# Optimization experiments

Measured on AMD Instinct MI355X. Metric: run time of the kernel, lower is better.

The kernel has to match this reference:

```python
import jax, jax.numpy as jnp
import numpy as np

B, H, W = 16, 512, 512
HW = H * W
K = 512  # max regions kept per image (compacted region list for jit)


def _ccl(mask):
    """8-connected component labeling on a (H,W) bool mask.
    Label = min flat pixel index of the component (matches skimage scan-order
    region ordering after compaction); background label = HW sentinel."""
    idx = jnp.arange(HW, dtype=jnp.int32).reshape(H, W)
    lab0 = jnp.where(mask, idx, HW)

    def body(c):
        l, _ = c
        p = jnp.pad(l, 1, constant_values=HW)
        m = l
        for dr in (-1, 0, 1):
            for dc in (-1, 0, 1):
                m = jnp.minimum(m, p[1 + dr:1 + dr + H, 1 + dc:1 + dc + W])
        nl = jnp.where(mask, m, HW)
        return nl, jnp.all(nl == l)

    lab, _ = jax.lax.while_loop(lambda c: ~c[1], body, (lab0, jnp.array(False)))
    return lab


def _pixel_errors(pred_m, gt_m):
    """Faithful vectorized version of TopoLoss.calculate_error for one image.
    All torch updates are max-semantics (set-to-1 or raise-to-error), so the
    final map is an elementwise max over region contributions."""
    pl = _ccl(pred_m).ravel()  # pred labels, bg = HW
    gl = _ccl(gt_m).ravel()    # gt labels, bg = HW
    ones = jnp.ones(HW, jnp.float32)
    rows = (jnp.arange(HW) // W).astype(jnp.float32)
    cols = (jnp.arange(HW) % W).astype(jnp.float32)
    seg = lambda v, l: jax.ops.segment_sum(v, l, num_segments=HW + 1)
    pa, psr, psc = seg(ones, pl), seg(rows, pl), seg(cols, pl)
    ga, gsr, gsc = seg(ones, gl), seg(rows, gl), seg(cols, gl)
    p_valid = pa[:HW] > 0
    g_valid = ga[:HW] > 0
    # compact region lists; stable argsort keeps ascending label order = scan order
    p_ids = jnp.argsort(jnp.where(p_valid, 0, 1))[:K]
    g_ids = jnp.argsort(jnp.where(g_valid, 0, 1))[:K]
    pv, gv = p_valid[p_ids], g_valid[g_ids]
    pA, gA = pa[p_ids], ga[g_ids]
    pcr, pcc = psr[p_ids] / jnp.maximum(pA, 1.0), psc[p_ids] / jnp.maximum(pA, 1.0)
    gcr, gcc = gsr[g_ids] / jnp.maximum(gA, 1.0), gsc[g_ids] / jnp.maximum(gA, 1.0)
    # nearest gt centroid per pred region (argmin ties -> first, as in torch loop)
    d2 = (pcr[:, None] - gcr[None, :]) ** 2 + (pcc[:, None] - gcc[None, :]) ** 2
    d2 = jnp.where(gv[None, :], d2, jnp.inf)
    nn = jnp.argmin(d2, axis=1)  # (K,) compact gt index
    ratio = 1.0 - gA[nn] / jnp.maximum(pA, 1.0)
    e = jnp.minimum(jnp.abs(1.0 - jnp.exp(ratio)), 1.0)
    gt_f = gt_m.astype(jnp.float32).ravel()
    pr_f = pred_m.astype(jnp.float32).ravel()
    # per-region overlap flags (check_overlap)
    ov_p = jax.ops.segment_max(gt_f, pl, num_segments=HW + 1) > 0
    ov_g = jax.ops.segment_max(pr_f, gl, num_segments=HW + 1) > 0
    has_gt = jnp.any(g_valid)
    e_eff = jnp.where(pv & ov_p[p_ids] & has_gt, e, 0.0)
    e_full = jnp.zeros(HW + 1, jnp.float32).at[p_ids].set(e_eff)
    # max error among overlapping pred regions matched to each gt region
    e_gt = jnp.maximum(
        jax.ops.segment_max(jnp.where(e_eff > 0, e_eff, -1.0), nn, num_segments=K), 0.0)
    e_gt_full = jnp.zeros(HW + 1, jnp.float32).at[g_ids].set(jnp.where(gv, e_gt, 0.0))
    in_p = pl < HW
    in_g = gl < HW
    err = jnp.where(in_p & ~has_gt, 1.0, 0.0)                                   # no gt regions
    err = jnp.where(in_p & has_gt & ~ov_p[pl], 1.0, err)                        # pred region w/o overlap
    err = jnp.maximum(err, jnp.where(in_p & has_gt & ov_p[pl] & (gt_f != 1.0),
                                     e_full[pl], 0.0))                          # pred pixels, gt!=1
    err = jnp.maximum(err, jnp.where(in_g & (pr_f < 1.0), e_gt_full[gl], 0.0))  # matched gt pixels, pred<1
    err = jnp.where(in_g & ~ov_g[gl], 1.0, err)                                 # gt region w/o overlap
    return err.reshape(H, W)


def _forward(inputs, target):
    score = jax.nn.sigmoid(inputs)  # forward() applies sigmoid before _topo_loss
    pred = score > 0.5
    gt = target > 0.5
    pe = jax.lax.stop_gradient(jax.vmap(_pixel_errors)(pred, gt))
    loss_map = (jax.nn.sigmoid((score + 1.0) * pe) - 0.5) * 2.0
    loss = jnp.mean(loss_map)
    m1 = 1.0 - jnp.mean(pe)
    m2 = 1.0 - jnp.sum(pe) / jnp.count_nonzero(pe).astype(jnp.float32)
    return loss, m1, m2


def setup_inputs() -> dict:
    key = jax.random.key(0)
    k1, k2 = jax.random.split(key)
    # low-frequency fields -> realistic blob regions after thresholding
    inputs = 3.0 * jax.image.resize(jax.random.normal(k1, (B, 16, 16)), (B, H, W), "cubic")
    target = (jax.image.resize(jax.random.normal(k2, (B, 16, 16)), (B, H, W), "cubic") > 0).astype(jnp.float32)
    return {"inputs": inputs, "target": target, "epoch": 1}


def reference(inputs, target, epoch):
    return _forward(inputs, target)
```

## Files before the change

kernel.cpp:

```cpp
#include <hip/hip_runtime.h>

#define NB 16
#define HH 512
#define WW 512
#define HWN (HH * WW)
#define SENT HWN
#define KC 512
#define RCAP 4096
#define CCAP 4096
#define PN (NB * HWN)
#define TPB 256
#define IMAX 0x7FFFFFFF
#define TS 64
#define TSQ (TS * TS)
#define NFIN (NB * 64)

typedef unsigned short ushortT;
typedef unsigned int uintT;
typedef unsigned long long ullT;

__device__ __forceinline__ int findRootL(int* s, int i) {
    int p = s[i];
    while (p != i) { i = p; p = s[i]; }
    return i;
}

__device__ __forceinline__ void uniteL(int* s, int a, int b) {
    int ra = findRootL(s, a);
    int rb = findRootL(s, b);
    while (ra != rb) {
        int lo = min(ra, rb), hi = max(ra, rb);
        int old = atomicMin(&s[hi], lo);
        if (old == hi) return;
        ra = old; rb = lo;
    }
}

__device__ __forceinline__ int rootPk(const int* __restrict__ par, int s) {
    int q = par[s];
    while ((q & (CCAP - 1)) != s) { s = q & (CCAP - 1); q = par[s]; }
    return q;
}

__device__ __forceinline__ void uniteS(int* par, int a, int b) {
    int pa = rootPk(par, a);
    int pb = rootPk(par, b);
    while (pa != pb) {
        int lo = min(pa, pb), hi = max(pa, pb);
        int hs = hi & (CCAP - 1);
        int old = atomicMin(&par[hs], lo);
        if (old == hi) return;
        pa = rootPk(par, old & (CCAP - 1));
        pb = rootPk(par, lo & (CCAP - 1));
    }
}

__device__ __forceinline__ int bsearch_k(const int* a, int key) {
    int lo = 0, hi = KC;
    while (lo < hi) { int m = (lo + hi) >> 1; if (a[m] < key) lo = m + 1; else hi = m; }
    return (lo < KC && a[lo] == key) ? lo : -1;
}

__global__ __launch_bounds__(TPB) void k_prep(const float* __restrict__ in, const float* __restrict__ tg,
                                              ullT* __restrict__ rmP, ullT* __restrict__ rmG) {
    int lane = threadIdx.x & 63;
    int wid = (blockIdx.x * blockDim.x + threadIdx.x) >> 6;
    const float4* in4 = (const float4*)in;
    const float4* tg4 = (const float4*)tg;
    #pragma unroll
    for (int it = 0; it < 2; it++) {
        int span = wid + (it << 13);
        int vidx = (span << 6) + lane;
        float4 a = in4[vidx];
        float4 t4 = tg4[vidx];
        uintT bp = (a.x > 0.0f) | ((a.y > 0.0f) << 1) | ((a.z > 0.0f) << 2) | ((a.w > 0.0f) << 3);
        uintT bg = (t4.x > 0.5f) | ((t4.y > 0.5f) << 1) | ((t4.z > 0.5f) << 2) | ((t4.w > 0.5f) << 3);
        ullT vp = (ullT)bp << ((lane & 15) << 2);
        ullT vg = (ullT)bg << ((lane & 15) << 2);
        #pragma unroll
        for (int o = 1; o < 16; o <<= 1) {
            vp |= __shfl_xor(vp, o);
            vg |= __shfl_xor(vg, o);
        }
        if ((lane & 15) == 0) {
            int g = (span << 8) + ((lane >> 4) << 6);
            int b = g >> 18, r = (g >> 9) & 511, tc = (g >> 6) & 7;
            int idx = (((tc << 4) + b) << 9) + r;
            rmP[idx] = vp; rmG[idx] = vg;
        }
    }
}

__global__ __launch_bounds__(TPB) void k_local(const ullT* __restrict__ rmPArr, const ullT* __restrict__ rmGArr,
                        ushortT* __restrict__ slotP, ushortT* __restrict__ slotG,
                        int* __restrict__ parP, int* __restrict__ parG,
                        ullT* __restrict__ cmLP, ullT* __restrict__ cmRP,
                        ullT* __restrict__ cmLG, ullT* __restrict__ cmRG,
                        int* __restrict__ candCntP, int* __restrict__ candCntG,
                        int* __restrict__ sAreaP, int* __restrict__ sRP, int* __restrict__ sCP, int* __restrict__ sOvP,
                        int* __restrict__ sAreaG, int* __restrict__ sRG, int* __restrict__ sCG, int* __restrict__ sOvG) {
    __shared__ int s[TSQ];
    __shared__ ullT rm[TS], rmO[TS];
    int side = blockIdx.x & 1;
    int tileIdx = blockIdx.x >> 1;
    int b = tileIdx >> 6;
    int tile = tileIdx & 63;
    int r0 = (tile >> 3) << 6, c0 = (tile & 7) << 6;
    int tc = tile & 7;
    int base = (b << 18) + (r0 << 9) + c0;
    int wv = threadIdx.x >> 6, lane = threadIdx.x & 63;

    const ullT* own = side ? rmGArr : rmPArr;
    const ullT* oth = side ? rmPArr : rmGArr;
    ushortT* slotArr = side ? slotG : slotP;
    int* par  = side ? parG : parP;
    ullT* cmLo = side ? cmLG : cmLP;
    ullT* cmRo = side ? cmRG : cmRP;
    int* candCnt = side ? candCntG : candCntP;
    int* sArea = side ? sAreaG : sAreaP;
    int* sR = side ? sRG : sRP;
    int* sC = side ? sCG : sCP;
    int* sOv = side ? sOvG : sOvP;

    int rowIdx = (((tc << 4) + b) << 9) + r0;
    if (threadIdx.x < 64) rm[threadIdx.x] = own[rowIdx + threadIdx.x];
    else if (threadIdx.x < 128) rmO[threadIdx.x - 64] = oth[rowIdx + threadIdx.x - 64];
    __syncthreads();

    if (threadIdx.x < 64) {
        ullT v = rm[threadIdx.x];
        ullT mL = __ballot((v & 1ULL) != 0);
        ullT mR = __ballot((v >> 63) != 0);
        if (threadIdx.x == 0) { cmLo[tileIdx] = mL; cmRo[tileIdx] = mR; }
    }

    #pragma unroll
    for (int k = 0; k < 16; k++) {
        int lr = wv + (k << 2);
        ullT mp = rm[lr];
        bool p = (mp >> lane) & 1ULL;
        int t = (lr << 6) + lane;
        ullT below = (lane == 0) ? 0ULL : ((~mp) & ((1ULL << lane) - 1ULL));
        int st = below ? (64 - __clzll(below)) : 0;
        s[t] = p ? ((lr << 6) + st) : TSQ;
    }
    __syncthreads();

    for (int lr = wv; lr < TS; lr += 4) {
        if (lr == 0) continue;
        int t = (lr << 6) + lane;
        ullT m = rm[lr], a = rm[lr - 1];
        if ((m >> lane) & 1ULL) {
            bool N  = (a >> lane) & 1ULL;
            bool W  = lane > 0  && ((m >> (lane - 1)) & 1ULL);
            bool NW = lane > 0  && ((a >> (lane - 1)) & 1ULL);
            bool E  = lane < 63 && ((m >> (lane + 1)) & 1ULL);
            bool NE = lane < 63 && ((a >> (lane + 1)) & 1ULL);
            if (N) { if (!(W && NW)) uniteL(s, t, t - TS); }
            else {
                if (NW && !W) uniteL(s, t, t - TS - 1);
                if (NE && !E) uniteL(s, t, t - TS + 1);
            }
        }
    }
    __syncthreads();

    #pragma unroll
    for (int k = 0; k < 16; k++) {
        int t = ((wv + (k << 2)) << 6) + lane;
        if (s[t] < TSQ) s[t] = findRootL(s, t);
    }
    __syncthreads();

    #pragma unroll
    for (int k = 0; k < 16; k++) {
        int t = ((wv + (k << 2)) << 6) + lane;
        if (s[t] == t) {
            int pos = atomicAdd(&candCnt[b], 1);
            if (pos >= CCAP) pos = CCAP - 1;
            int gl = ((r0 + (t >> 6)) << 9) + (c0 + (t & 63));
            par[b * CCAP + pos] = (gl << 12) | pos;
            s[t] = -(pos + 2);
        }
    }
    __syncthreads();

    #pragma unroll
    for (int k = 0; k < 16; k++) {
        int lr = wv + (k << 2);
        int t = (lr << 6) + lane;
        int g = base + (lr << 9) + lane;
        int vp = s[t];
        int slot = 0;
        if (vp != TSQ) slot = (vp < 0) ? (-vp - 1) : (-s[vp] - 1);
        slotArr[g] = (ushortT)slot;
        ullT mp = rm[lr], mq = rmO[lr];
        bool isF = (mp >> lane) & 1ULL;
        if (isF && (lane == 0 || !((mp >> (lane - 1)) & 1ULL))) {
            ullT x = ~(mp >> lane);
            int len = x ? (__ffsll((long long)x) - 1) : (64 - lane);
            int sl = slot - 1;
            ullT runbits = (len >= 64) ? ~0ULL : (((1ULL << len) - 1ULL) << lane);
            atomicAdd(&sArea[b * CCAP + sl], len);
            atomicAdd(&sR[b * CCAP + sl], (r0 + lr) * len);
            atomicAdd(&sC[b * CCAP + sl], len * (c0 + lane) + (len * (len - 1)) / 2);
            if (mq & runbits) atomicOr(&sOv[b * CCAP + sl], 1);
        }
    }
}

__global__ __launch_bounds__(TPB) void k_bmerge(
        const ullT* __restrict__ rmP, const ullT* __restrict__ rmG,
        const ullT* __restrict__ cmLP, const ullT* __restrict__ cmRP,
        const ullT* __restrict__ cmLG, const ullT* __restrict__ cmRG,
        const ushortT* __restrict__ slotP, const ushortT* __restrict__ slotG,
        int* __restrict__ parP, int* __restrict__ parG) {
    int wid = (blockIdx.x << 2) + (threadIdx.x >> 6);
    int lane = threadIdx.x & 63;
    int b = wid / 168;
    int rem = wid % 168;
    int type = rem / 56;
    int sub = rem % 56;
    int q = sub >> 3, t8 = sub & 7;

    for (int side = 0; side < 2; side++) {
        const ullT* rm = side ? rmG : rmP;
        const ullT* cmL = side ? cmLG : cmLP;
        const ullT* cmR = side ? cmRG : cmRP;
        const ushortT* S = (side ? slotG : slotP) + (b << 18);
        int* par = (side ? parG : parP) + b * CCAP;

        if (type == 0) {
            int r = (q + 1) << 6, tc = t8;
            int ib = (((tc << 4) + b) << 9);
            ullT m = rm[ib + r];
            if (!m) continue;
            ullT a = rm[ib + r - 1];
            ullT mW = 0, aW = 0, mE = 0, aE = 0;
            if (tc > 0) { int iw = ((((tc - 1) << 4) + b) << 9); mW = rm[iw + r]; aW = rm[iw + r - 1]; }
            if (tc < 7) { int ie = ((((tc + 1) << 4) + b) << 9); mE = rm[ie + r]; aE = rm[ie + r - 1]; }
            if ((m >> lane) & 1ULL) {
                bool N  = (a >> lane) & 1ULL;
                bool W  = lane ? ((m >> (lane - 1)) & 1ULL) : ((mW >> 63) & 1ULL);
                bool NW = lane ? ((a >> (lane - 1)) & 1ULL) : ((aW >> 63) & 1ULL);
                bool E  = (lane < 63) ? ((m >> (lane + 1)) & 1ULL) : (mE & 1ULL);
                bool NE = (lane < 63) ? ((a >> (lane + 1)) & 1ULL) : (aE & 1ULL);
                int i = (r << 9) + (tc << 6) + lane;
                if (N) {
                    if (!(W && NW)) uniteS(par, S[i] - 1, S[i - WW] - 1);
                } else {
                    if (NW && !W) uniteS(par, S[i] - 1, S[i - WW - 1] - 1);
                    if (NE && !E) uniteS(par, S[i] - 1, S[i - WW + 1] - 1);
                }
            }
        } else if (type == 1) {
            int c = (q + 1) << 6, tr = t8;
            int ownT = (b << 6) + (tr << 3) + (q + 1);
            int wstT = ownT - 1;
            ullT co = cmL[ownT];
            if (!co) continue;
            ullT cw = cmR[wstT];
            ullT coA = 0, cwA = 0;
            if (tr > 0) { coA = cmL[ownT - 8]; cwA = cmR[wstT - 8]; }
            int r = lane;
            if ((co >> r) & 1ULL) {
                bool W  = (cw >> r) & 1ULL;
                bool pO = r ? ((co >> (r - 1)) & 1ULL) : ((coA >> 63) & 1ULL);
                bool pW = r ? ((cw >> (r - 1)) & 1ULL) : ((cwA >> 63) & 1ULL);
                int i = (((tr << 6) + r) << 9) + c;
                if (r == 0) {
                    if (W) uniteS(par, S[i] - 1, S[i - 1] - 1);
                    else if (pW) uniteS(par, S[i] - 1, S[i - WW - 1] - 1);
                } else {
                    if (W) { if (!(pO && pW)) uniteS(par, S[i] - 1, S[i - 1] - 1); }
                    else if (pW && !pO) uniteS(par, S[i] - 1, S[i - WW - 1] - 1);
                }
            }
        } else {
            int c = (q << 6) + 63, tr = t8;
            int ownT = (b << 6) + (tr << 3) + q;
            int estT = ownT + 1;
            ullT co = cmR[ownT];
            if (!co) continue;
            ullT ce = cmL[estT];
            ullT coA = 0, ceA = 0;
            if (tr > 0) { coA = cmR[ownT - 8]; ceA = cmL[estT - 8]; }
            int r = lane;
            if ((co >> r) & 1ULL) {
                bool E  = (ce >> r) & 1ULL;
                bool NE = r ? ((ce >> (r - 1)) & 1ULL) : ((ceA >> 63) & 1ULL);
                bool pO = r ? ((co >> (r - 1)) & 1ULL) : false;
                if (NE && !E && !pO) {
                    int i = (((tr << 6) + r) << 9) + c;
                    uniteS(par, S[i] - 1, S[i - WW + 1] - 1);
                }
            }
        }
    }
}

__global__ __launch_bounds__(512) void k_post(
        const int* __restrict__ parP, const int* __restrict__ parG,
        const int* __restrict__ candCntP, const int* __restrict__ candCntG,
        const int* __restrict__ sAreaP, const int* __restrict__ sRP, const int* __restrict__ sCP, const int* __restrict__ sOvP,
        const int* __restrict__ sAreaG, const int* __restrict__ sRG, const int* __restrict__ sCG, const int* __restrict__ sOvG,
        int* __restrict__ ccntG_g, float* __restrict__ vPs, float* __restrict__ vGs) {
    __shared__ int s[RCAP];
    __shared__ int compL[2][KC];
    __shared__ int stA[2][KC], stR[2][KC], stC[2][KC], stOv[2][KC];
    __shared__ float gAf[KC], gRf[KC], gCf[KC], sEG[KC], sFPl[KC], sFGl[KC];
    __shared__ int lcnt, ccX[2];
    int b = blockIdx.x;
    int tid = threadIdx.x;

    for (int side = 0; side < 2; side++) {
        const int* par = (side ? parG : parP) + b * CCAP;
        int n = min((side ? candCntG : candCntP)[b], CCAP);
        if (tid == 0) lcnt = 0;
        __syncthreads();
        for (int t = tid; t < n; t += 512) {
            int pk = par[t];
            if ((pk & (CCAP - 1)) == t) { int pos = atomicAdd(&lcnt, 1); if (pos < RCAP) s[pos] = pk >> 12; }
        }
        __syncthreads();
        int nn2 = min(lcnt, RCAP);
        int m = 1; while (m < nn2) m <<= 1;
        for (int t = nn2 + tid; t < m; t += 512) s[t] = IMAX;
        __syncthreads();
        for (int k = 2; k <= m; k <<= 1) {
            for (int j = k >> 1; j > 0; j >>= 1) {
                for (int t = tid; t < m; t += 512) {
                    int ixj = t ^ j;
                    if (ixj > t) {
                        int a = s[t], bb = s[ixj];
                        bool up = ((t & k) == 0);
                        if ((a > bb) == up) { s[t] = bb; s[ixj] = a; }
                    }
                }
                __syncthreads();
            }
        }
        int cc = min(nn2, KC);
        for (int t = tid; t < KC; t += 512)
            compL[side][t] = (t < cc) ? s[t] : IMAX;
        if (tid == 0) { ccX[side] = cc; if (side) ccntG_g[b] = cc; }
        __syncthreads();
    }

    for (int t = tid; t < KC; t += 512) {
        stA[0][t] = 0; stR[0][t] = 0; stC[0][t] = 0; stOv[0][t] = 0;
        stA[1][t] = 0; stR[1][t] = 0; stC[1][t] = 0; stOv[1][t] = 0;
    }
    __syncthreads();

    short* cidS = (short*)s;
    for (int side = 0; side < 2; side++) {
        const int* par = (side ? parG : parP) + b * CCAP;
        const int* aA = side ? sAreaG : sAreaP;
        const int* aR = side ? sRG : sRP;
        const int* aC = side ? sCG : sCP;
        const int* aO = side ? sOvG : sOvP;
        int n = min((side ? candCntG : candCntP)[b], CCAP);
        for (int slot = tid; slot < n; slot += 512) {
            int pk = rootPk(par, slot);
            int cid = bsearch_k(compL[side], pk >> 12);
            cidS[side * CCAP + slot] = (short)cid;
            if (cid >= 0) {
                int sidx = b * CCAP + slot;
                atomicAdd(&stA[side][cid], aA[sidx]);
                atomicAdd(&stR[side][cid], aR[sidx]);
                atomicAdd(&stC[side][cid], aC[sidx]);
                if (aO[sidx]) atomicOr(&stOv[side][cid], 1);
            }
        }
    }
    __syncthreads();

    int t = tid;
    int ccg = ccX[1], ccp = ccX[0];
    {
        float fa = (float)stA[1][t];
        float d = fmaxf(fa, 1.0f);
        gAf[t] = fa;
        gRf[t] = (float)stR[1][t] / d;
        gCf[t] = (float)stC[1][t] / d;
        sEG[t] = 0.0f;
    }
    __syncthreads();
    float e_eff = 0.0f;
    int nn = 0;
    if (t < ccp) {
        float pa = (float)stA[0][t];
        float dd = fmaxf(pa, 1.0f);
        float pcr = (float)stR[0][t] / dd;
        float pcc = (float)stC[0][t] / dd;
        float best = INFINITY;
        for (int gi = 0; gi < ccg; gi++) {
            float dr = pcr - gRf[gi], dc = pcc - gCf[gi];
            float d2 = dr * dr + dc * dc;
            if (d2 < best) { best = d2; nn = gi; }
        }
        if (ccg > 0 && stOv[0][t]) {
            float ratio = 1.0f - gAf[nn] / dd;
            e_eff = fminf(fabsf(1.0f - __expf(ratio)), 1.0f);
        }
    }
    if (e_eff > 0.0f) atomicMax((int*)&sEG[nn], __float_as_int(e_eff));
    sFPl[t] = stOv[0][t] ? e_eff : -1.0f;
    __syncthreads();
    sFGl[t] = stOv[1][t] ? fmaxf(sEG[t], 0.0f) : -1.0f;
// ... 85 lines not shown
    }
    int wv = threadIdx.x >> 6, lane = threadIdx.x & 63;
    if (lane == 0) { pLm[wv] = aLm; pPe[wv] = aPe; pCnt[wv] = aCnt; }
    __syncthreads();
    if (threadIdx.x == 0) {
        double sl = 0, sp = 0; int sc = 0;
        for (int q = 0; q < 4; q++) { sl += pLm[q]; sp += pPe[q]; sc += pCnt[q]; }
        partLm[blockIdx.x] = sl;
        partPe[blockIdx.x] = sp;
        partCnt[blockIdx.x] = (double)sc;
    }
}

__global__ __launch_bounds__(TPB) void k_out(const double* __restrict__ partLm,
                                             const double* __restrict__ partPe,
                                             const double* __restrict__ partCnt,
                                             float* __restrict__ out) {
    __shared__ double r0[TPB], r1[TPB], r2[TPB];
    double sl = 0, sp = 0, sc = 0;
    for (int i = threadIdx.x; i < NFIN; i += TPB) {
        sl += partLm[i]; sp += partPe[i]; sc += partCnt[i];
    }
    r0[threadIdx.x] = sl; r1[threadIdx.x] = sp; r2[threadIdx.x] = sc;
    __syncthreads();
    for (int s = TPB >> 1; s > 0; s >>= 1) {
        if (threadIdx.x < s) {
            r0[threadIdx.x] += r0[threadIdx.x + s];
            r1[threadIdx.x] += r1[threadIdx.x + s];
            r2[threadIdx.x] += r2[threadIdx.x + s];
        }
        __syncthreads();
    }
    if (threadIdx.x == 0) {
        out[0] = (float)(r0[0] / (double)PN);
        out[1] = (float)(1.0 - r1[0] / (double)PN);
        out[2] = (float)(1.0 - r1[0] / r2[0]);
    }
}

extern "C" void kernel_launch(void* const* d_in, const int* in_sizes, int n_in,
                              void* d_out, int out_size, void* d_ws, size_t ws_size,
                              hipStream_t stream) {
    const float* in = (const float*)d_in[0];
    const float* tg = (const float*)d_in[1];

    char* w = (char*)d_ws;
    size_t off = 0;
    ullT* rmP = (ullT*)(w + off); off += (size_t)(PN / 64) * 8;
    ullT* rmG = (ullT*)(w + off); off += (size_t)(PN / 64) * 8;
    ushortT* slotP = (ushortT*)(w + off); off += (size_t)PN * 2;
    ushortT* slotG = (ushortT*)(w + off); off += (size_t)PN * 2;
    int* parP = (int*)(w + off); off += (size_t)NB * CCAP * 4;
    int* parG = (int*)(w + off); off += (size_t)NB * CCAP * 4;
    ullT* cmLP = (ullT*)(w + off); off += (size_t)NB * 64 * 8;
    ullT* cmRP = (ullT*)(w + off); off += (size_t)NB * 64 * 8;
    ullT* cmLG = (ullT*)(w + off); off += (size_t)NB * 64 * 8;
    ullT* cmRG = (ullT*)(w + off); off += (size_t)NB * 64 * 8;
    float* vPs = (float*)(w + off); off += (size_t)NB * CCAP * 4;
    float* vGs = (float*)(w + off); off += (size_t)NB * CCAP * 4;
    int* ccntG = (int*)(w + off); off += NB * 4;
    double* partLm = (double*)(w + off); off += (size_t)NFIN * 8;
    double* partPe = (double*)(w + off); off += (size_t)NFIN * 8;
    double* partCnt = (double*)(w + off); off += (size_t)NFIN * 8;
    size_t zoff = off;
    int* candCntP = (int*)(w + off); off += NB * 4;
    int* candCntG = (int*)(w + off); off += NB * 4;
    int* sAreaP = (int*)(w + off); off += (size_t)NB * CCAP * 4;
    int* sRP    = (int*)(w + off); off += (size_t)NB * CCAP * 4;
    int* sCP    = (int*)(w + off); off += (size_t)NB * CCAP * 4;
    int* sOvP   = (int*)(w + off); off += (size_t)NB * CCAP * 4;
    int* sAreaG = (int*)(w + off); off += (size_t)NB * CCAP * 4;
    int* sRG    = (int*)(w + off); off += (size_t)NB * CCAP * 4;
    int* sCG    = (int*)(w + off); off += (size_t)NB * CCAP * 4;
    int* sOvG   = (int*)(w + off); off += (size_t)NB * CCAP * 4;
    size_t zend = off;

    hipMemsetAsync(w + zoff, 0, zend - zoff, stream);

    k_prep<<<2048, TPB, 0, stream>>>(in, tg, rmP, rmG);
    k_local<<<NB * 64 * 2, TPB, 0, stream>>>(rmP, rmG, slotP, slotG, parP, parG,
                                             cmLP, cmRP, cmLG, cmRG,
                                             candCntP, candCntG,
                                             sAreaP, sRP, sCP, sOvP,
                                             sAreaG, sRG, sCG, sOvG);
    k_bmerge<<<672, TPB, 0, stream>>>(rmP, rmG, cmLP, cmRP, cmLG, cmRG,
                                      slotP, slotG, parP, parG);
    k_post<<<NB, 512, 0, stream>>>(parP, parG, candCntP, candCntG,
                                   sAreaP, sRP, sCP, sOvP,
                                   sAreaG, sRG, sCG, sOvG,
                                   ccntG, vPs, vGs);
    k_final<<<NFIN, TPB, 0, stream>>>(in, slotP, slotG, vPs, vGs, ccntG,
                                      partLm, partPe, partCnt);
    k_out<<<1, TPB, 0, stream>>>(partLm, partPe, partCnt, (float*)d_out);
}
```

Baseline: 134.7 us.

## Halve local CCL tile height to 32x64 and extend boundary merge accordingly

Local connected-component labeling now runs on 32-row by 64-column tiles instead of 64x64. That doubles the block count of the local kernel and halves its shared-memory footprint, which is meant to raise occupancy and parallelism. The boundary-merge kernel is rewritten for 15 horizontal seams and 16 tile rows per column seam. The trade-off is more seams to merge, more component candidates and more global union-find atomics in the merge and post stages.

```diff
diff --git a/kernel.cpp b/kernel.cpp
--- a/kernel.cpp
+++ b/kernel.cpp
@@ -11,8 +11,7 @@
 #define PN (NB * HWN)
 #define TPB 256
 #define IMAX 0x7FFFFFFF
-#define TS 64
-#define TSQ (TS * TS)
+#define TSQ2 2048
 #define NFIN (NB * 64)
 
 typedef unsigned short ushortT;
@@ -99,14 +98,14 @@
                         int* __restrict__ candCntP, int* __restrict__ candCntG,
                         int* __restrict__ sAreaP, int* __restrict__ sRP, int* __restrict__ sCP, int* __restrict__ sOvP,
                         int* __restrict__ sAreaG, int* __restrict__ sRG, int* __restrict__ sCG, int* __restrict__ sOvG) {
-    __shared__ int s[TSQ];
-    __shared__ ullT rm[TS], rmO[TS];
+    __shared__ int s[TSQ2];
+    __shared__ ullT rm[32], rmO[32];
     int side = blockIdx.x & 1;
-    int tileIdx = blockIdx.x >> 1;
-    int b = tileIdx >> 6;
-    int tile = tileIdx & 63;
-    int r0 = (tile >> 3) << 6, c0 = (tile & 7) << 6;
-    int tc = tile & 7;
+    int segIdx = blockIdx.x >> 1;
+    int b = segIdx >> 7;
+    int seg = segIdx & 127;
+    int tr = seg >> 3, tc = seg & 7;
+    int r0 = tr << 5, c0 = tc << 6;
     int base = (b << 18) + (r0 << 9) + c0;
     int wv = threadIdx.x >> 6, lane = threadIdx.x & 63;
 
@@ -123,30 +122,35 @@
     int* sOv = side ? sOvG : sOvP;
 
     int rowIdx = (((tc << 4) + b) << 9) + r0;
-    if (threadIdx.x < 64) rm[threadIdx.x] = own[rowIdx + threadIdx.x];
-    else if (threadIdx.x < 128) rmO[threadIdx.x - 64] = oth[rowIdx + threadIdx.x - 64];
+    if (threadIdx.x < 32) rm[threadIdx.x] = own[rowIdx + threadIdx.x];
+    else if (threadIdx.x < 64) rmO[threadIdx.x - 32] = oth[rowIdx + threadIdx.x - 32];
     __syncthreads();
 
     if (threadIdx.x < 64) {
-        ullT v = rm[threadIdx.x];
+        ullT v = (threadIdx.x < 32) ? rm[threadIdx.x] : 0ULL;
         ullT mL = __ballot((v & 1ULL) != 0);
         ullT mR = __ballot((v >> 63) != 0);
-        if (threadIdx.x == 0) { cmLo[tileIdx] = mL; cmRo[tileIdx] = mR; }
-    }
-
-    #pragma unroll
-    for (int k = 0; k < 16; k++) {
+        if (threadIdx.x == 0) {
+            int ci = (b << 7) + seg;
+            cmLo[ci] = mL; cmRo[ci] = mR;
+        }
+    }
+
+    #pragma unroll
+    for (int k = 0; k < 8; k++) {
         int lr = wv + (k << 2);
         ullT mp = rm[lr];
         bool p = (mp >> lane) & 1ULL;
         int t = (lr << 6) + lane;
         ullT below = (lane == 0) ? 0ULL : ((~mp) & ((1ULL << lane) - 1ULL));
         int st = below ? (64 - __clzll(below)) : 0;
-        s[t] = p ? ((lr << 6) + st) : TSQ;
-    }
-    __syncthreads();
-
-    for (int lr = wv; lr < TS; lr += 4) {
+        s[t] = p ? ((lr << 6) + st) : TSQ2;
+    }
+    __syncthreads();
+
+    #pragma unroll
+    for (int k = 0; k < 8; k++) {
+        int lr = wv + (k << 2);
         if (lr == 0) continue;
         int t = (lr << 6) + lane;
         ullT m = rm[lr], a = rm[lr - 1];
@@ -156,24 +160,24 @@
             bool NW = lane > 0  && ((a >> (lane - 1)) & 1ULL);
             bool E  = lane < 63 && ((m >> (lane + 1)) & 1ULL);
             bool NE = lane < 63 && ((a >> (lane + 1)) & 1ULL);
-            if (N) { if (!(W && NW)) uniteL(s, t, t - TS); }
+            if (N) { if (!(W && NW)) uniteL(s, t, t - 64); }
             else {
-                if (NW && !W) uniteL(s, t, t - TS - 1);
-                if (NE && !E) uniteL(s, t, t - TS + 1);
-            }
-        }
-    }
-    __syncthreads();
-
-    #pragma unroll
-    for (int k = 0; k < 16; k++) {
+                if (NW && !W) uniteL(s, t, t - 64 - 1);
+                if (NE && !E) uniteL(s, t, t - 64 + 1);
+            }
+        }
+    }
+    __syncthreads();
+
+    #pragma unroll
+    for (int k = 0; k < 8; k++) {
         int t = ((wv + (k << 2)) << 6) + lane;
-        if (s[t] < TSQ) s[t] = findRootL(s, t);
-    }
-    __syncthreads();
-
-    #pragma unroll
-    for (int k = 0; k < 16; k++) {
+        if (s[t] < TSQ2) s[t] = findRootL(s, t);
+    }
+    __syncthreads();
+
+    #pragma unroll
+    for (int k = 0; k < 8; k++) {
         int t = ((wv + (k << 2)) << 6) + lane;
         if (s[t] == t) {
             int pos = atomicAdd(&candCnt[b], 1);
@@ -186,13 +190,13 @@
     __syncthreads();
 
     #pragma unroll
-    for (int k = 0; k < 16; k++) {
+    for (int k = 0; k < 8; k++) {
         int lr = wv + (k << 2);
         int t = (lr << 6) + lane;
         int g = base + (lr << 9) + lane;
         int vp = s[t];
         int slot = 0;
-        if (vp != TSQ) slot = (vp < 0) ? (-vp - 1) : (-s[vp] - 1);
+        if (vp != TSQ2) slot = (vp < 0) ? (-vp - 1) : (-s[vp] - 1);
         slotArr[g] = (ushortT)slot;
         ullT mp = rm[lr], mq = rmO[lr];
         bool isF = (mp >> lane) & 1ULL;
@@ -217,11 +221,9 @@
         int* __restrict__ parP, int* __restrict__ parG) {
     int wid = (blockIdx.x << 2) + (threadIdx.x >> 6);
     int lane = threadIdx.x & 63;
-    int b = wid / 168;
-    int rem = wid % 168;
-    int type = rem / 56;
-    int sub = rem % 56;
-    int q = sub >> 3, t8 = sub & 7;
+    if (wid >= NB * 344) return;
+    int b = wid / 344;
+    int rem = wid % 344;
 
     for (int side = 0; side < 2; side++) {
         const ullT* rm = side ? rmG : rmP;
@@ -230,8 +232,9 @@
         const ushortT* S = (side ? slotG : slotP) + (b << 18);
         int* par = (side ? parG : parP) + b * CCAP;
 
-        if (type == 0) {
-            int r = (q + 1) << 6, tc = t8;
+        if (rem < 120) {
+            int q = rem >> 3, tc = rem & 7;
+            int r = (q + 1) << 5;
             int ib = (((tc << 4) + b) << 9);
             ullT m = rm[ib + r];
             if (!m) continue;
@@ -253,45 +256,48 @@
                     if (NE && !E) uniteS(par, S[i] - 1, S[i - WW + 1] - 1);
                 }
             }
-        } else if (type == 1) {
-            int c = (q + 1) << 6, tr = t8;
-            int ownT = (b << 6) + (tr << 3) + (q + 1);
+        } else if (rem < 232) {
+            int u = rem - 120;
+            int q = u >> 4, tr = u & 15;
+            int c = (q + 1) << 6;
+            int ownT = (b << 7) + (tr << 3) + (q + 1);
             int wstT = ownT - 1;
             ullT co = cmL[ownT];
             if (!co) continue;
             ullT cw = cmR[wstT];
-            ullT coA = 0, cwA = 0;
-            if (tr > 0) { coA = cmL[ownT - 8]; cwA = cmR[wstT - 8]; }
+            ullT cwA = (tr > 0) ? cmR[wstT - 8] : 0ULL;
             int r = lane;
             if ((co >> r) & 1ULL) {
-                bool W  = (cw >> r) & 1ULL;
-                bool pO = r ? ((co >> (r - 1)) & 1ULL) : ((coA >> 63) & 1ULL);
-                bool pW = r ? ((cw >> (r - 1)) & 1ULL) : ((cwA >> 63) & 1ULL);
-                int i = (((tr << 6) + r) << 9) + c;
+                bool W = (cw >> r) & 1ULL;
+                int i = (((tr << 5) + r) << 9) + c;
                 if (r == 0) {
+                    bool pW = (cwA >> 31) & 1ULL;
                     if (W) uniteS(par, S[i] - 1, S[i - 1] - 1);
                     else if (pW) uniteS(par, S[i] - 1, S[i - WW - 1] - 1);
                 } else {
+                    bool pO = (co >> (r - 1)) & 1ULL;
+                    bool pW = (cw >> (r - 1)) & 1ULL;
                     if (W) { if (!(pO && pW)) uniteS(par, S[i] - 1, S[i - 1] - 1); }
                     else if (pW && !pO) uniteS(par, S[i] - 1, S[i - WW - 1] - 1);
                 }
             }
         } else {
-            int c = (q << 6) + 63, tr = t8;
-            int ownT = (b << 6) + (tr << 3) + q;
+            int u = rem - 232;
+            int q = u >> 4, tr = u & 15;
+            int c = (q << 6) + 63;
+            int ownT = (b << 7) + (tr << 3) + q;
             int estT = ownT + 1;
             ullT co = cmR[ownT];
             if (!co) continue;
             ullT ce = cmL[estT];
-            ullT coA = 0, ceA = 0;
-            if (tr > 0) { coA = cmR[ownT - 8]; ceA = cmL[estT - 8]; }
+            ullT ceA = (tr > 0) ? cmL[estT - 8] : 0ULL;
             int r = lane;
             if ((co >> r) & 1ULL) {
                 bool E  = (ce >> r) & 1ULL;
-                bool NE = r ? ((ce >> (r - 1)) & 1ULL) : ((ceA >> 63) & 1ULL);
+                bool NE = r ? ((ce >> (r - 1)) & 1ULL) : ((ceA >> 31) & 1ULL);
                 bool pO = r ? ((co >> (r - 1)) & 1ULL) : false;
                 if (NE && !E && !pO) {
-                    int i = (((tr << 6) + r) << 9) + c;
+                    int i = (((tr << 5) + r) << 9) + c;
                     uniteS(par, S[i] - 1, S[i - WW + 1] - 1);
                 }
             }
@@ -547,10 +553,10 @@
     ushortT* slotG = (ushortT*)(w + off); off += (size_t)PN * 2;
     int* parP = (int*)(w + off); off += (size_t)NB * CCAP * 4;
     int* parG = (int*)(w + off); off += (size_t)NB * CCAP * 4;
-    ullT* cmLP = (ullT*)(w + off); off += (size_t)NB * 64 * 8;
-    ullT* cmRP = (ullT*)(w + off); off += (size_t)NB * 64 * 8;
-    ullT* cmLG = (ullT*)(w + off); off += (size_t)NB * 64 * 8;
-    ullT* cmRG = (ullT*)(w + off); off += (size_t)NB * 64 * 8;
+    ullT* cmLP = (ullT*)(w + off); off += (size_t)NB * 128 * 8;
+    ullT* cmRP = (ullT*)(w + off); off += (size_t)NB * 128 * 8;
+    ullT* cmLG = (ullT*)(w + off); off += (size_t)NB * 128 * 8;
+    ullT* cmRG = (ullT*)(w + off); off += (size_t)NB * 128 * 8;
     float* vPs = (float*)(w + off); off += (size_t)NB * CCAP * 4;
     float* vGs = (float*)(w + off); off += (size_t)NB * CCAP * 4;
     int* ccntG = (int*)(w + off); off += NB * 4;
@@ -573,13 +579,16 @@
     hipMemsetAsync(w + zoff, 0, zend - zoff, stream);
 
     k_prep<<<2048, TPB, 0, stream>>>(in, tg, rmP, rmG);
-    k_local<<<NB * 64 * 2, TPB, 0, stream>>>(rmP, rmG, slotP, slotG, parP, parG,
-                                             cmLP, cmRP, cmLG, cmRG,
-                                             candCntP, candCntG,
-                                             sAreaP, sRP, sCP, sOvP,
-                                             sAreaG, sRG, sCG, sOvG);
-    k_bmerge<<<672, TPB, 0, stream>>>(rmP, rmG, cmLP, cmRP, cmLG, cmRG,
-                                      slotP, slotG, parP, parG);
+    k_local<<<NB * 128 * 2, TPB, 0, stream>>>(rmP, rmG, slotP, slotG, parP, parG,
+                                              cmLP, cmRP, cmLG, cmRG,
+                                              candCntP, candCntG,
+                                              sAreaP, sRP, sCP, sOvP,
+                                              sAreaG, sRG, sCG, sOvG);
+    {
+        const int totalWaves = NB * 344;
+        k_bmerge<<<(totalWaves + 3) / 4, TPB, 0, stream>>>(rmP, rmG, cmLP, cmRP, cmLG, cmRG,
+                                                           slotP, slotG, parP, parG);
+    }
     k_post<<<NB, 512, 0, stream>>>(parP, parG, candCntP, candCntG,
                                    sAreaP, sRP, sCP, sOvP,
                                    sAreaG, sRG, sCG, sOvG,
```

Result: slower. 145.1 us (+7.7%).

## Fuse mask packing into k_local and boundary merge into k_post with LDS union-find

Applied to the files above, without the earlier changes.

The separate prep kernel is removed. k_local now thresholds the raw float inputs directly, using wave ballots to build per-row bitmasks, and writes the packed rows out for later use. The tile-boundary merge kernel is folded into k_post, which copies each image's parent arrays into shared memory and runs the unions there. Two launches and the global-memory atomics on the parent arrays go away. The catch is that boundary merging now runs in only 16 blocks (one per image) instead of 672, so that phase has much less parallelism.

```diff
diff --git a/kernel.cpp b/kernel.cpp
--- a/kernel.cpp
+++ b/kernel.cpp
@@ -4,7 +4,6 @@
 #define HH 512
 #define WW 512
 #define HWN (HH * WW)
-#define SENT HWN
 #define KC 512
 #define RCAP 4096
 #define CCAP 4096
@@ -36,7 +35,7 @@
     }
 }
 
-__device__ __forceinline__ int rootPk(const int* __restrict__ par, int s) {
+__device__ __forceinline__ int rootPk(const int* par, int s) {
     int q = par[s];
     while ((q & (CCAP - 1)) != s) { s = q & (CCAP - 1); q = par[s]; }
     return q;
@@ -61,39 +60,10 @@
     return (lo < KC && a[lo] == key) ? lo : -1;
 }
 
-__global__ __launch_bounds__(TPB) void k_prep(const float* __restrict__ in, const float* __restrict__ tg,
-                                              ullT* __restrict__ rmP, ullT* __restrict__ rmG) {
-    int lane = threadIdx.x & 63;
-    int wid = (blockIdx.x * blockDim.x + threadIdx.x) >> 6;
-    const float4* in4 = (const float4*)in;
-    const float4* tg4 = (const float4*)tg;
-    #pragma unroll
-    for (int it = 0; it < 2; it++) {
-        int span = wid + (it << 13);
-        int vidx = (span << 6) + lane;
-        float4 a = in4[vidx];
-        float4 t4 = tg4[vidx];
-        uintT bp = (a.x > 0.0f) | ((a.y > 0.0f) << 1) | ((a.z > 0.0f) << 2) | ((a.w > 0.0f) << 3);
-        uintT bg = (t4.x > 0.5f) | ((t4.y > 0.5f) << 1) | ((t4.z > 0.5f) << 2) | ((t4.w > 0.5f) << 3);
-        ullT vp = (ullT)bp << ((lane & 15) << 2);
-        ullT vg = (ullT)bg << ((lane & 15) << 2);
-        #pragma unroll
-        for (int o = 1; o < 16; o <<= 1) {
-            vp |= __shfl_xor(vp, o);
-            vg |= __shfl_xor(vg, o);
-        }
-        if ((lane & 15) == 0) {
-            int g = (span << 8) + ((lane >> 4) << 6);
-            int b = g >> 18, r = (g >> 9) & 511, tc = (g >> 6) & 7;
-            int idx = (((tc << 4) + b) << 9) + r;
-            rmP[idx] = vp; rmG[idx] = vg;
-        }
-    }
-}
-
-__global__ __launch_bounds__(TPB) void k_local(const ullT* __restrict__ rmPArr, const ullT* __restrict__ rmGArr,
+__global__ __launch_bounds__(TPB) void k_local(const float* __restrict__ in, const float* __restrict__ tg,
                         ushortT* __restrict__ slotP, ushortT* __restrict__ slotG,
                         int* __restrict__ parP, int* __restrict__ parG,
+                        ullT* __restrict__ rmPArr, ullT* __restrict__ rmGArr,
                         ullT* __restrict__ cmLP, ullT* __restrict__ cmRP,
                         ullT* __restrict__ cmLG, ullT* __restrict__ cmRG,
                         int* __restrict__ candCntP, int* __restrict__ candCntG,
@@ -110,10 +80,13 @@
     int base = (b << 18) + (r0 << 9) + c0;
     int wv = threadIdx.x >> 6, lane = threadIdx.x & 63;
 
-    const ullT* own = side ? rmGArr : rmPArr;
-    const ullT* oth = side ? rmPArr : rmGArr;
+    const float* own = side ? tg : in;
+    const float* oth = side ? in : tg;
+    const float ownThr = side ? 0.5f : 0.0f;
+    const float othThr = side ? 0.0f : 0.5f;
     ushortT* slotArr = side ? slotG : slotP;
     int* par  = side ? parG : parP;
+    ullT* rmOut = side ? rmGArr : rmPArr;
     ullT* cmLo = side ? cmLG : cmLP;
     ullT* cmRo = side ? cmRG : cmRP;
     int* candCnt = side ? candCntG : candCntP;
@@ -122,13 +95,20 @@
     int* sC = side ? sCG : sCP;
     int* sOv = side ? sOvG : sOvP;
 
-    int rowIdx = (((tc << 4) + b) << 9) + r0;
-    if (threadIdx.x < 64) rm[threadIdx.x] = own[rowIdx + threadIdx.x];
-    else if (threadIdx.x < 128) rmO[threadIdx.x - 64] = oth[rowIdx + threadIdx.x - 64];
+    #pragma unroll
+    for (int k = 0; k < 16; k++) {
+        int lr = wv + (k << 2);
+        int gg = base + (lr << 9) + lane;
+        ullT mp = __ballot(own[gg] > ownThr);
+        ullT mq = __ballot(oth[gg] > othThr);
+        if (lane == 0) { rm[lr] = mp; rmO[lr] = mq; }
+    }
     __syncthreads();
 
     if (threadIdx.x < 64) {
         ullT v = rm[threadIdx.x];
+        int rowIdx = (((tc << 4) + b) << 9) + r0;
+        rmOut[rowIdx + threadIdx.x] = v;
         ullT mL = __ballot((v & 1ULL) != 0);
         ullT mR = __ballot((v >> 63) != 0);
         if (threadIdx.x == 0) { cmLo[tileIdx] = mL; cmRo[tileIdx] = mR; }
@@ -209,102 +189,17 @@
     }
 }
 
-__global__ __launch_bounds__(TPB) void k_bmerge(
+__global__ __launch_bounds__(512) void k_post(
         const ullT* __restrict__ rmP, const ullT* __restrict__ rmG,
         const ullT* __restrict__ cmLP, const ullT* __restrict__ cmRP,
         const ullT* __restrict__ cmLG, const ullT* __restrict__ cmRG,
         const ushortT* __restrict__ slotP, const ushortT* __restrict__ slotG,
-        int* __restrict__ parP, int* __restrict__ parG) {
-    int wid = (blockIdx.x << 2) + (threadIdx.x >> 6);
-    int lane = threadIdx.x & 63;
-    int b = wid / 168;
-    int rem = wid % 168;
-    int type = rem / 56;
-    int sub = rem % 56;
-    int q = sub >> 3, t8 = sub & 7;
-
-    for (int side = 0; side < 2; side++) {
-        const ullT* rm = side ? rmG : rmP;
-        const ullT* cmL = side ? cmLG : cmLP;
-        const ullT* cmR = side ? cmRG : cmRP;
-        const ushortT* S = (side ? slotG : slotP) + (b << 18);
-        int* par = (side ? parG : parP) + b * CCAP;
-
-        if (type == 0) {
-            int r = (q + 1) << 6, tc = t8;
-            int ib = (((tc << 4) + b) << 9);
-            ullT m = rm[ib + r];
-            if (!m) continue;
-            ullT a = rm[ib + r - 1];
-            ullT mW = 0, aW = 0, mE = 0, aE = 0;
-            if (tc > 0) { int iw = ((((tc - 1) << 4) + b) << 9); mW = rm[iw + r]; aW = rm[iw + r - 1]; }
-            if (tc < 7) { int ie = ((((tc + 1) << 4) + b) << 9); mE = rm[ie + r]; aE = rm[ie + r - 1]; }
-            if ((m >> lane) & 1ULL) {
-                bool N  = (a >> lane) & 1ULL;
-                bool W  = lane ? ((m >> (lane - 1)) & 1ULL) : ((mW >> 63) & 1ULL);
-                bool NW = lane ? ((a >> (lane - 1)) & 1ULL) : ((aW >> 63) & 1ULL);
-                bool E  = (lane < 63) ? ((m >> (lane + 1)) & 1ULL) : (mE & 1ULL);
-                bool NE = (lane < 63) ? ((a >> (lane + 1)) & 1ULL) : (aE & 1ULL);
-                int i = (r << 9) + (tc << 6) + lane;
-                if (N) {
-                    if (!(W && NW)) uniteS(par, S[i] - 1, S[i - WW] - 1);
-                } else {
-                    if (NW && !W) uniteS(par, S[i] - 1, S[i - WW - 1] - 1);
-                    if (NE && !E) uniteS(par, S[i] - 1, S[i - WW + 1] - 1);
-                }
-            }
-        } else if (type == 1) {
-            int c = (q + 1) << 6, tr = t8;
-            int ownT = (b << 6) + (tr << 3) + (q + 1);
-            int wstT = ownT - 1;
-            ullT co = cmL[ownT];
-            if (!co) continue;
-            ullT cw = cmR[wstT];
-            ullT coA = 0, cwA = 0;
-            if (tr > 0) { coA = cmL[ownT - 8]; cwA = cmR[wstT - 8]; }
-            int r = lane;
-            if ((co >> r) & 1ULL) {
-                bool W  = (cw >> r) & 1ULL;
-                bool pO = r ? ((co >> (r - 1)) & 1ULL) : ((coA >> 63) & 1ULL);
-                bool pW = r ? ((cw >> (r - 1)) & 1ULL) : ((cwA >> 63) & 1ULL);
-                int i = (((tr << 6) + r) << 9) + c;
-                if (r == 0) {
-                    if (W) uniteS(par, S[i] - 1, S[i - 1] - 1);
-                    else if (pW) uniteS(par, S[i] - 1, S[i - WW - 1] - 1);
-                } else {
-                    if (W) { if (!(pO && pW)) uniteS(par, S[i] - 1, S[i - 1] - 1); }
-                    else if (pW && !pO) uniteS(par, S[i] - 1, S[i - WW - 1] - 1);
-                }
-            }
-        } else {
-            int c = (q << 6) + 63, tr = t8;
-            int ownT = (b << 6) + (tr << 3) + q;
-            int estT = ownT + 1;
-            ullT co = cmR[ownT];
-            if (!co) continue;
-            ullT ce = cmL[estT];
-            ullT coA = 0, ceA = 0;
-            if (tr > 0) { coA = cmR[ownT - 8]; ceA = cmL[estT - 8]; }
-            int r = lane;
-            if ((co >> r) & 1ULL) {
-                bool E  = (ce >> r) & 1ULL;
-                bool NE = r ? ((ce >> (r - 1)) & 1ULL) : ((ceA >> 63) & 1ULL);
-                bool pO = r ? ((co >> (r - 1)) & 1ULL) : false;
-                if (NE && !E && !pO) {
-                    int i = (((tr << 6) + r) << 9) + c;
-                    uniteS(par, S[i] - 1, S[i - WW + 1] - 1);
-                }
-            }
-        }
-    }
-}
-
-__global__ __launch_bounds__(512) void k_post(
         const int* __restrict__ parP, const int* __restrict__ parG,
         const int* __restrict__ candCntP, const int* __restrict__ candCntG,
         const int* __restrict__ sAreaP, const int* __restrict__ sRP, const int* __restrict__ sCP, const int* __restrict__ sOvP,
         const int* __restrict__ sAreaG, const int* __restrict__ sRG, const int* __restrict__ sCG, const int* __restrict__ sOvG,
         int* __restrict__ ccntG_g, float* __restrict__ vPs, float* __restrict__ vGs) {
+    __shared__ int parL[2][CCAP];
     __shared__ int s[RCAP];
     __shared__ int compL[2][KC];
     __shared__ int stA[2][KC], stR[2][KC], stC[2][KC], stOv[2][KC];
@@ -312,9 +207,97 @@
     __shared__ int lcnt, ccX[2];
     int b = blockIdx.x;
     int tid = threadIdx.x;
+    int wv8 = tid >> 6, lane = tid & 63;
+
+    for (int t = tid; t < CCAP; t += 512) {
+        parL[0][t] = parP[b * CCAP + t];
+        parL[1][t] = parG[b * CCAP + t];
+    }
+    __syncthreads();
+
+    for (int task = wv8; task < 168; task += 8) {
+        int type = task / 56;
+        int sub = task % 56;
+        int q = sub >> 3, t8 = sub & 7;
+        for (int side = 0; side < 2; side++) {
+            const ullT* rm = side ? rmG : rmP;
+            const ullT* cmL = side ? cmLG : cmLP;
+            const ullT* cmR = side ? cmRG : cmRP;
+            const ushortT* S = (side ? slotG : slotP) + (b << 18);
+            int* par = parL[side];
+
+            if (type == 0) {
+                int r = (q + 1) << 6, tc = t8;
+                int ib = (((tc << 4) + b) << 9);
+                ullT m = rm[ib + r];
+                if (!m) continue;
+                ullT a = rm[ib + r - 1];
+                ullT mW = 0, aW = 0, mE = 0, aE = 0;
+                if (tc > 0) { int iw = ((((tc - 1) << 4) + b) << 9); mW = rm[iw + r]; aW = rm[iw + r - 1]; }
+                if (tc < 7) { int ie = ((((tc + 1) << 4) + b) << 9); mE = rm[ie + r]; aE = rm[ie + r - 1]; }
+                if ((m >> lane) & 1ULL) {
+                    bool N  = (a >> lane) & 1ULL;
+                    bool W  = lane ? ((m >> (lane - 1)) & 1ULL) : ((mW >> 63) & 1ULL);
+                    bool NW = lane ? ((a >> (lane - 1)) & 1ULL) : ((aW >> 63) & 1ULL);
+                    bool E  = (lane < 63) ? ((m >> (lane + 1)) & 1ULL) : (mE & 1ULL);
+                    bool NE = (lane < 63) ? ((a >> (lane + 1)) & 1ULL) : (aE & 1ULL);
+                    int i = (r << 9) + (tc << 6) + lane;
+                    if (N) {
+                        if (!(W && NW)) uniteS(par, S[i] - 1, S[i - WW] - 1);
+                    } else {
+                        if (NW && !W) uniteS(par, S[i] - 1, S[i - WW - 1] - 1);
+                        if (NE && !E) uniteS(par, S[i] - 1, S[i - WW + 1] - 1);
+                    }
+                }
+            } else if (type == 1) {
+                int c = (q + 1) << 6, tr = t8;
+                int ownT = (b << 6) + (tr << 3) + (q + 1);
+                int wstT = ownT - 1;
+                ullT co = cmL[ownT];
+                if (!co) continue;
+                ullT cw = cmR[wstT];
+                ullT coA = 0, cwA = 0;
+                if (tr > 0) { coA = cmL[ownT - 8]; cwA = cmR[wstT - 8]; }
+                int r = lane;
+                if ((co >> r) & 1ULL) {
+                    bool W  = (cw >> r) & 1ULL;
+                    bool pO = r ? ((co >> (r - 1)) & 1ULL) : ((coA >> 63) & 1ULL);
+                    bool pW = r ? ((cw >> (r - 1)) & 1ULL) : ((cwA >> 63) & 1ULL);
+                    int i = (((tr << 6) + r) << 9) + c;
+                    if (r == 0) {
+                        if (W) uniteS(par, S[i] - 1, S[i - 1] - 1);
+                        else if (pW) uniteS(par, S[i] - 1, S[i - WW - 1] - 1);
+                    } else {
+                        if (W) { if (!(pO && pW)) uniteS(par, S[i] - 1, S[i - 1] - 1); }
+                        else if (pW && !pO) uniteS(par, S[i] - 1, S[i - WW - 1] - 1);
+                    }
+                }
+            } else {
+                int c = (q << 6) + 63, tr = t8;
+                int ownT = (b << 6) + (tr << 3) + q;
+                int estT = ownT + 1;
+                ullT co = cmR[ownT];
+                if (!co) continue;
+                ullT ce = cmL[estT];
+                ullT coA = 0, ceA = 0;
+                if (tr > 0) { coA = cmR[ownT - 8]; ceA = cmL[estT - 8]; }
+                int r = lane;
+                if ((co >> r) & 1ULL) {
+                    bool E  = (ce >> r) & 1ULL;
+                    bool NE = r ? ((ce >> (r - 1)) & 1ULL) : ((ceA >> 63) & 1ULL);
+                    bool pO = r ? ((co >> (r - 1)) & 1ULL) : false;
+                    if (NE && !E && !pO) {
+                        int i = (((tr << 6) + r) << 9) + c;
+                        uniteS(par, S[i] - 1, S[i - WW + 1] - 1);
+                    }
+                }
+            }
+        }
+    }
+    __syncthreads();
 
     for (int side = 0; side < 2; side++) {
-        const int* par = (side ? parG : parP) + b * CCAP;
+        const int* par = parL[side];
         int n = min((side ? candCntG : candCntP)[b], CCAP);
         if (tid == 0) lcnt = 0;
         __syncthreads();
@@ -355,7 +338,7 @@
 
     short* cidS = (short*)s;
     for (int side = 0; side < 2; side++) {
-        const int* par = (side ? parG : parP) + b * CCAP;
+        const int* par = parL[side];
         const int* aA = side ? sAreaG : sAreaP;
         const int* aR = side ? sRG : sRP;
         const int* aC = side ? sCG : sCP;
@@ -572,15 +555,14 @@
 
     hipMemsetAsync(w + zoff, 0, zend - zoff, stream);
 
-    k_prep<<<2048, TPB, 0, stream>>>(in, tg, rmP, rmG);
-    k_local<<<NB * 64 * 2, TPB, 0, stream>>>(rmP, rmG, slotP, slotG, parP, parG,
-                                             cmLP, cmRP, cmLG, cmRG,
+    k_local<<<NB * 64 * 2, TPB, 0, stream>>>(in, tg, slotP, slotG, parP, parG,
+                                             rmP, rmG, cmLP, cmRP, cmLG, cmRG,
                                              candCntP, candCntG,
                                              sAreaP, sRP, sCP, sOvP,
                                              sAreaG, sRG, sCG, sOvG);
-    k_bmerge<<<672, TPB, 0, stream>>>(rmP, rmG, cmLP, cmRP, cmLG, cmRG,
-                                      slotP, slotG, parP, parG);
-    k_post<<<NB, 512, 0, stream>>>(parP, parG, candCntP, candCntG,
+    k_post<<<NB, 512, 0, stream>>>(rmP, rmG, cmLP, cmRP, cmLG, cmRG,
+                                   slotP, slotG, parP, parG,
+                                   candCntP, candCntG,
                                    sAreaP, sRP, sCP, sOvP,
                                    sAreaG, sRG, sCG, sOvG,
                                    ccntG, vPs, vGs);
```

New measurement: 177.6 us. 31.9% more time.

## Fuse boundary merge into post kernel using shared-memory union-find

Applied to the files above, without the earlier changes.

Removes the separate k_bmerge launch and performs the tile-boundary union operations inside k_post. Each block loads its image's parent arrays into LDS and runs the union-find merges there with LDS atomics before the compaction and sort. This saves a kernel launch and global-memory atomics. The cost is that the merge work now runs on only 16 blocks with 8 waves each, instead of 672 blocks, and LDS usage grows by 32KB.

```diff
diff --git a/kernel.cpp b/kernel.cpp
--- a/kernel.cpp
+++ b/kernel.cpp
@@ -4,7 +4,6 @@
 #define HH 512
 #define WW 512
 #define HWN (HH * WW)
-#define SENT HWN
 #define KC 512
 #define RCAP 4096
 #define CCAP 4096
@@ -36,7 +35,7 @@
     }
 }
 
-__device__ __forceinline__ int rootPk(const int* __restrict__ par, int s) {
+__device__ __forceinline__ int rootPk(const int* par, int s) {
     int q = par[s];
     while ((q & (CCAP - 1)) != s) { s = q & (CCAP - 1); q = par[s]; }
     return q;
@@ -209,102 +208,17 @@
     }
 }
 
-__global__ __launch_bounds__(TPB) void k_bmerge(
+__global__ __launch_bounds__(512) void k_post(
         const ullT* __restrict__ rmP, const ullT* __restrict__ rmG,
         const ullT* __restrict__ cmLP, const ullT* __restrict__ cmRP,
         const ullT* __restrict__ cmLG, const ullT* __restrict__ cmRG,
         const ushortT* __restrict__ slotP, const ushortT* __restrict__ slotG,
-        int* __restrict__ parP, int* __restrict__ parG) {
-    int wid = (blockIdx.x << 2) + (threadIdx.x >> 6);
-    int lane = threadIdx.x & 63;
-    int b = wid / 168;
-    int rem = wid % 168;
-    int type = rem / 56;
-    int sub = rem % 56;
-    int q = sub >> 3, t8 = sub & 7;
-
-    for (int side = 0; side < 2; side++) {
-        const ullT* rm = side ? rmG : rmP;
-        const ullT* cmL = side ? cmLG : cmLP;
-        const ullT* cmR = side ? cmRG : cmRP;
-        const ushortT* S = (side ? slotG : slotP) + (b << 18);
-        int* par = (side ? parG : parP) + b * CCAP;
-
-        if (type == 0) {
-            int r = (q + 1) << 6, tc = t8;
-            int ib = (((tc << 4) + b) << 9);
-            ullT m = rm[ib + r];
-            if (!m) continue;
-            ullT a = rm[ib + r - 1];
-            ullT mW = 0, aW = 0, mE = 0, aE = 0;
-            if (tc > 0) { int iw = ((((tc - 1) << 4) + b) << 9); mW = rm[iw + r]; aW = rm[iw + r - 1]; }
-            if (tc < 7) { int ie = ((((tc + 1) << 4) + b) << 9); mE = rm[ie + r]; aE = rm[ie + r - 1]; }
-            if ((m >> lane) & 1ULL) {
-                bool N  = (a >> lane) & 1ULL;
-                bool W  = lane ? ((m >> (lane - 1)) & 1ULL) : ((mW >> 63) & 1ULL);
-                bool NW = lane ? ((a >> (lane - 1)) & 1ULL) : ((aW >> 63) & 1ULL);
-                bool E  = (lane < 63) ? ((m >> (lane + 1)) & 1ULL) : (mE & 1ULL);
-                bool NE = (lane < 63) ? ((a >> (lane + 1)) & 1ULL) : (aE & 1ULL);
-                int i = (r << 9) + (tc << 6) + lane;
-                if (N) {
-                    if (!(W && NW)) uniteS(par, S[i] - 1, S[i - WW] - 1);
-                } else {
-                    if (NW && !W) uniteS(par, S[i] - 1, S[i - WW - 1] - 1);
-                    if (NE && !E) uniteS(par, S[i] - 1, S[i - WW + 1] - 1);
-                }
-            }
-        } else if (type == 1) {
-            int c = (q + 1) << 6, tr = t8;
-            int ownT = (b << 6) + (tr << 3) + (q + 1);
-            int wstT = ownT - 1;
-            ullT co = cmL[ownT];
-            if (!co) continue;
-            ullT cw = cmR[wstT];
-            ullT coA = 0, cwA = 0;
-            if (tr > 0) { coA = cmL[ownT - 8]; cwA = cmR[wstT - 8]; }
-            int r = lane;
-            if ((co >> r) & 1ULL) {
-                bool W  = (cw >> r) & 1ULL;
-                bool pO = r ? ((co >> (r - 1)) & 1ULL) : ((coA >> 63) & 1ULL);
-                bool pW = r ? ((cw >> (r - 1)) & 1ULL) : ((cwA >> 63) & 1ULL);
-                int i = (((tr << 6) + r) << 9) + c;
-                if (r == 0) {
-                    if (W) uniteS(par, S[i] - 1, S[i - 1] - 1);
-                    else if (pW) uniteS(par, S[i] - 1, S[i - WW - 1] - 1);
-                } else {
-                    if (W) { if (!(pO && pW)) uniteS(par, S[i] - 1, S[i - 1] - 1); }
-                    else if (pW && !pO) uniteS(par, S[i] - 1, S[i - WW - 1] - 1);
-                }
-            }
-        } else {
-            int c = (q << 6) + 63, tr = t8;
-            int ownT = (b << 6) + (tr << 3) + q;
-            int estT = ownT + 1;
-            ullT co = cmR[ownT];
-            if (!co) continue;
-            ullT ce = cmL[estT];
-            ullT coA = 0, ceA = 0;
-            if (tr > 0) { coA = cmR[ownT - 8]; ceA = cmL[estT - 8]; }
-            int r = lane;
-            if ((co >> r) & 1ULL) {
-                bool E  = (ce >> r) & 1ULL;
-                bool NE = r ? ((ce >> (r - 1)) & 1ULL) : ((ceA >> 63) & 1ULL);
-                bool pO = r ? ((co >> (r - 1)) & 1ULL) : false;
-                if (NE && !E && !pO) {
-                    int i = (((tr << 6) + r) << 9) + c;
-                    uniteS(par, S[i] - 1, S[i - WW + 1] - 1);
-                }
-            }
-        }
-    }
-}
-
-__global__ __launch_bounds__(512) void k_post(
         const int* __restrict__ parP, const int* __restrict__ parG,
         const int* __restrict__ candCntP, const int* __restrict__ candCntG,
         const int* __restrict__ sAreaP, const int* __restrict__ sRP, const int* __restrict__ sCP, const int* __restrict__ sOvP,
         const int* __restrict__ sAreaG, const int* __restrict__ sRG, const int* __restrict__ sCG, const int* __restrict__ sOvG,
         int* __restrict__ ccntG_g, float* __restrict__ vPs, float* __restrict__ vGs) {
+    __shared__ int parL[2][CCAP];
     __shared__ int s[RCAP];
     __shared__ int compL[2][KC];
     __shared__ int stA[2][KC], stR[2][KC], stC[2][KC], stOv[2][KC];
@@ -312,9 +226,97 @@
     __shared__ int lcnt, ccX[2];
     int b = blockIdx.x;
     int tid = threadIdx.x;
+    int wv8 = tid >> 6, lane = tid & 63;
+
+    for (int t = tid; t < CCAP; t += 512) {
+        parL[0][t] = parP[b * CCAP + t];
+        parL[1][t] = parG[b * CCAP + t];
+    }
+    __syncthreads();
+
+    for (int task = wv8; task < 168; task += 8) {
+        int type = task / 56;
+        int sub = task % 56;
+        int q = sub >> 3, t8 = sub & 7;
+        for (int side = 0; side < 2; side++) {
+            const ullT* rm = side ? rmG : rmP;
+            const ullT* cmL = side ? cmLG : cmLP;
+            const ullT* cmR = side ? cmRG : cmRP;
+            const ushortT* S = (side ? slotG : slotP) + (b << 18);
+            int* par = parL[side];
+
+            if (type == 0) {
+                int r = (q + 1) << 6, tc = t8;
+                int ib = (((tc << 4) + b) << 9);
+                ullT m = rm[ib + r];
+                if (!m) continue;
+                ullT a = rm[ib + r - 1];
+                ullT mW = 0, aW = 0, mE = 0, aE = 0;
+                if (tc > 0) { int iw = ((((tc - 1) << 4) + b) << 9); mW = rm[iw + r]; aW = rm[iw + r - 1]; }
+                if (tc < 7) { int ie = ((((tc + 1) << 4) + b) << 9); mE = rm[ie + r]; aE = rm[ie + r - 1]; }
+                if ((m >> lane) & 1ULL) {
+                    bool N  = (a >> lane) & 1ULL;
+                    bool W  = lane ? ((m >> (lane - 1)) & 1ULL) : ((mW >> 63) & 1ULL);
+                    bool NW = lane ? ((a >> (lane - 1)) & 1ULL) : ((aW >> 63) & 1ULL);
+                    bool E  = (lane < 63) ? ((m >> (lane + 1)) & 1ULL) : (mE & 1ULL);
+                    bool NE = (lane < 63) ? ((a >> (lane + 1)) & 1ULL) : (aE & 1ULL);
+                    int i = (r << 9) + (tc << 6) + lane;
+                    if (N) {
+                        if (!(W && NW)) uniteS(par, S[i] - 1, S[i - WW] - 1);
+                    } else {
+                        if (NW && !W) uniteS(par, S[i] - 1, S[i - WW - 1] - 1);
+                        if (NE && !E) uniteS(par, S[i] - 1, S[i - WW + 1] - 1);
+                    }
+                }
+            } else if (type == 1) {
+                int c = (q + 1) << 6, tr = t8;
+                int ownT = (b << 6) + (tr << 3) + (q + 1);
+                int wstT = ownT - 1;
+                ullT co = cmL[ownT];
+                if (!co) continue;
+                ullT cw = cmR[wstT];
+                ullT coA = 0, cwA = 0;
+                if (tr > 0) { coA = cmL[ownT - 8]; cwA = cmR[wstT - 8]; }
+                int r = lane;
+                if ((co >> r) & 1ULL) {
+                    bool W  = (cw >> r) & 1ULL;
+                    bool pO = r ? ((co >> (r - 1)) & 1ULL) : ((coA >> 63) & 1ULL);
+                    bool pW = r ? ((cw >> (r - 1)) & 1ULL) : ((cwA >> 63) & 1ULL);
+                    int i = (((tr << 6) + r) << 9) + c;
+                    if (r == 0) {
+                        if (W) uniteS(par, S[i] - 1, S[i - 1] - 1);
+                        else if (pW) uniteS(par, S[i] - 1, S[i - WW - 1] - 1);
+                    } else {
+                        if (W) { if (!(pO && pW)) uniteS(par, S[i] - 1, S[i - 1] - 1); }
+                        else if (pW && !pO) uniteS(par, S[i] - 1, S[i - WW - 1] - 1);
+                    }
+                }
+            } else {
+                int c = (q << 6) + 63, tr = t8;
+                int ownT = (b << 6) + (tr << 3) + q;
+                int estT = ownT + 1;
+                ullT co = cmR[ownT];
+                if (!co) continue;
+                ullT ce = cmL[estT];
+                ullT coA = 0, ceA = 0;
+                if (tr > 0) { coA = cmR[ownT - 8]; ceA = cmL[estT - 8]; }
+                int r = lane;
+                if ((co >> r) & 1ULL) {
+                    bool E  = (ce >> r) & 1ULL;
+                    bool NE = r ? ((ce >> (r - 1)) & 1ULL) : ((ceA >> 63) & 1ULL);
+                    bool pO = r ? ((co >> (r - 1)) & 1ULL) : false;
+                    if (NE && !E && !pO) {
+                        int i = (((tr << 6) + r) << 9) + c;
+                        uniteS(par, S[i] - 1, S[i - WW + 1] - 1);
+                    }
+                }
+            }
+        }
+    }
+    __syncthreads();
 
     for (int side = 0; side < 2; side++) {
-        const int* par = (side ? parG : parP) + b * CCAP;
+        const int* par = parL[side];
         int n = min((side ? candCntG : candCntP)[b], CCAP);
         if (tid == 0) lcnt = 0;
         __syncthreads();
@@ -355,7 +357,7 @@
 
     short* cidS = (short*)s;
     for (int side = 0; side < 2; side++) {
-        const int* par = (side ? parG : parP) + b * CCAP;
+        const int* par = parL[side];
         const int* aA = side ? sAreaG : sAreaP;
         const int* aR = side ? sRG : sRP;
         const int* aC = side ? sCG : sCP;
@@ -578,9 +580,9 @@
                                              candCntP, candCntG,
                                              sAreaP, sRP, sCP, sOvP,
                                              sAreaG, sRG, sCG, sOvG);
-    k_bmerge<<<672, TPB, 0, stream>>>(rmP, rmG, cmLP, cmRP, cmLG, cmRG,
-                                      slotP, slotG, parP, parG);
-    k_post<<<NB, 512, 0, stream>>>(parP, parG, candCntP, candCntG,
+    k_post<<<NB, 512, 0, stream>>>(rmP, rmG, cmLP, cmRP, cmLG, cmRG,
+                                   slotP, slotG, parP, parG,
+                                   candCntP, candCntG,
                                    sAreaP, sRP, sCP, sOvP,
                                    sAreaG, sRG, sCG, sOvG,
                                    ccntG, vPs, vGs);
```

After: 161.2 us. 19.7% more time.
